# Kernel tuning notes

Measured on AMD Instinct MI355X. Metric: run time of the kernel, lower is better.

## Reference

```python
import jax, jax.numpy as jnp
import numpy as np

B, N, F, H = 2, 256, 64, 4
HID = 64            # hidden_features
C = H * HID         # n_coefficients = 256
KF = 50             # kernel_features (rbf count)
CUTOFF_UPPER = 5.0  # ExpNormalSmearing default (lower = 0)
ALPHA = 5.0 / CUTOFF_UPPER


def _dense(key, din, dout):
    scale = 1.0 / np.sqrt(din)
    return jax.random.uniform(key, (din, dout), minval=-scale, maxval=scale).astype(jnp.float32)


def setup_inputs() -> dict:
    key = jax.random.key(0)
    ks = jax.random.split(key, 16)
    start = float(np.exp(-CUTOFF_UPPER))
    means = jnp.asarray(np.linspace(start, 1.0, KF), jnp.float32)
    betas = jnp.full((KF,), (2.0 / KF * (1.0 - start)) ** -2, dtype=jnp.float32)
    d_edge_in = 2 * F              # h_cat_ht width
    d_cat = 2 * F + KF + 1         # concat([h0, rbf*h, dist])
    return dict(
        h=jax.random.normal(ks[0], (B, N, F), jnp.float32),
        x=jax.random.normal(ks[1], (B, N, 3), jnp.float32),
        v=jax.random.normal(ks[2], (B, N, 3), jnp.float32) * 0.1,
        W_in=_dense(ks[3], d_edge_in, KF), b_in=jnp.zeros((KF,), jnp.float32),
        rbf_means=means, rbf_betas=betas,
        W_o1=_dense(ks[4], d_cat, HID), b_o1=jnp.zeros((HID,), jnp.float32),
        W_o2=_dense(ks[5], HID, HID), b_o2=jnp.zeros((HID,), jnp.float32),
        W_sem=_dense(ks[6], HID, H), b_sem=jnp.zeros((H,), jnp.float32),
        W_xmix=_dense(ks[7], C, C),
        W_p1=_dense(ks[8], C, HID), b_p1=jnp.zeros((HID,), jnp.float32),
        W_p2=_dense(ks[9], HID, HID), b_p2=jnp.zeros((HID,), jnp.float32),
        W_n1=_dense(ks[10], F + C + HID, HID), b_n1=jnp.zeros((HID,), jnp.float32),
        W_n2=_dense(ks[11], HID, F), b_n2=jnp.zeros((F,), jnp.float32),
        W_v1=_dense(ks[12], F, HID), b_v1=jnp.zeros((HID,), jnp.float32),
        W_v2=_dense(ks[13], HID, 1),
        W_vmix=_dense(ks[14], C, 1),
    )


def reference(h, x, v, W_in, b_in, rbf_means, rbf_betas, W_o1, b_o1, W_o2, b_o2,
              W_sem, b_sem, W_xmix, W_p1, b_p1, W_p2, b_p2,
              W_n1, b_n1, W_n2, b_n2, W_v1, b_v1, W_v2, W_vmix):
    silu = jax.nn.silu
    n = h.shape[-2]
    # all-pairs displacements: entry [i, j] = x_j - x_i  (get_x_minus_xt)
    x_minus_xt = x[..., None, :, :] - x[..., :, None, :]                       # [B,N,N,3]
    d = jnp.sqrt(jax.nn.relu((x_minus_xt ** 2).sum(-1, keepdims=True)) + 1e-5)  # [B,N,N,1]
    # h_cat_ht: concat([h_j, h_i]) per pair (get_h_cat_ht)
    h_j = jnp.broadcast_to(h[..., None, :, :], h.shape[:-2] + (n, n, h.shape[-1]))
    h_i = jnp.broadcast_to(h[..., :, None, :], h.shape[:-2] + (n, n, h.shape[-1]))
    h_cat = jnp.concatenate([h_j, h_i], -1)                                     # [B,N,N,2F]
    # --- edge model: ContinuousFilterConvolutionWithConcatenation ---
    h1 = h_cat @ W_in + b_in                                                    # [B,N,N,KF]
    cut = 0.5 * (jnp.cos(d * jnp.pi / CUTOFF_UPPER) + 1.0) * (d < CUTOFF_UPPER)
    rbf = cut * jnp.exp(-rbf_betas * (jnp.exp(-ALPHA * d) - rbf_means) ** 2)    # [B,N,N,KF]
    h_e_mtx = silu(jnp.concatenate([h_cat, rbf * h1, d], -1) @ W_o1 + b_o1) @ W_o2 + b_o2  # [B,N,N,HID]
    # --- semantic attention (cutoff=None => euclidean factor is 1.0) ---
    att = jax.nn.celu(h_e_mtx @ W_sem + b_sem, alpha=2.0)                       # [B,N,N,H]
    att = att - 1e5 * jnp.eye(n, dtype=att.dtype)[..., None]                    # mask self-pairs
    att = jax.nn.softmax(att, axis=-2)
    combined = att / att.sum(-2, keepdims=True)                                 # combined_attention
    # per-head weighted edge features, flattened (feature-major, head-minor)
    h_e_att = (h_e_mtx[..., :, None] * combined[..., None, :]).reshape(h_e_mtx.shape[:-1] + (C,))  # [B,N,N,C]
    # --- spatial attention ---
    coeff = jnp.tanh(h_e_att @ W_xmix)                                          # x_mixing, [B,N,N,C]
    x_hat = x_minus_xt / (d + 1e-5)                                             # [B,N,N,3]
    # combinations[b,i,j,c,:] = x_hat[b,i,j,:] * coeff[b,i,j,c]; mean over j, fused:
    comb_sum = jnp.einsum('bijc,bijd->bicd', coeff, x_hat) / n                  # [B,N,C,3]
    comb_norm = (comb_sum ** 2).sum(-1)                                         # [B,N,C]
    h_comb = silu(silu(comb_norm @ W_p1 + b_p1) @ W_p2 + b_p2)                  # post_norm_mlp
    # --- aggregate + node model (residual) ---
    h_e = h_e_att.sum(-2)                                                       # [B,N,C]
    h_new = h + silu(silu(jnp.concatenate([h, h_e, h_comb], -1) @ W_n1 + b_n1) @ W_n2 + b_n2)
    # --- velocity / coordinate update (v_mixing then mean over j, fused via comb_sum) ---
    delta_v = jnp.einsum('bicd,c->bid', comb_sum, W_vmix[:, 0])                 # [B,N,3]
    v_scale = 2.0 * jax.nn.sigmoid(silu(h_new @ W_v1 + b_v1) @ W_v2)            # velocity_mlp + double_sigmoid
    v_new = delta_v + v_scale * v
    x_new = x + v_new
    return (h_new, x_new, v_new)
```

## Files before the change

### kernel.cpp

```cpp
#include <hip/hip_runtime.h>
#include <hip/hip_bf16.h>

typedef __hip_bfloat16 bf16;
typedef __attribute__((ext_vector_type(8))) short bf16x8;
typedef __attribute__((ext_vector_type(4))) short s16x4;
typedef __attribute__((ext_vector_type(4))) float f32x4;

#define NNODE 512

__device__ __forceinline__ float b2f(bf16 v){ return __bfloat162float(v); }
__device__ __forceinline__ float siluf(float x){ return x / (1.f + __expf(-x)); }
__device__ __forceinline__ float tanhfast(float x){ return 1.f - 2.f/(__expf(2.f*x)+1.f); }
__device__ __forceinline__ float celu2(float x){ return x > 0.f ? x : 2.f*(__expf(0.5f*x)-1.f); }
__device__ __forceinline__ float bs2f(short v){ union{unsigned int i; float f;} t; t.i = ((unsigned int)(unsigned short)v) << 16; return t.f; }
__device__ __forceinline__ short f2bs(float x){ union{ bf16 b; short s; } u; u.b = __float2bfloat16(x); return u.s; }
__device__ __forceinline__ float lo16f(unsigned int u){ union{unsigned int i; float f;} t; t.i = u<<16; return t.f; }
__device__ __forceinline__ float hi16f(unsigned int u){ union{unsigned int i; float f;} t; t.i = u & 0xffff0000u; return t.f; }

template<typename T> __device__ __forceinline__ float ldv(const void* p, int i);
template<> __device__ __forceinline__ float ldv<float>(const void* p, int i){ return ((const float*)p)[i]; }
template<> __device__ __forceinline__ float ldv<bf16 >(const void* p, int i){ return b2f(((const bf16*)p)[i]); }

template<typename T> __device__ __forceinline__ void stv(void* p, int i, float v);
template<> __device__ __forceinline__ void stv<float>(void* p, int i, float v){ ((float*)p)[i] = v; }
template<> __device__ __forceinline__ void stv<bf16 >(void* p, int i, float v){ ((bf16*)p)[i] = __float2bfloat16(v); }

template<typename T> __device__ __forceinline__ short ldbs(const void* p, int i);
template<> __device__ __forceinline__ short ldbs<bf16 >(const void* p, int i){ union{ bf16 b; short s; } u; u.b = ((const bf16*)p)[i]; return u.s; }
template<> __device__ __forceinline__ short ldbs<float>(const void* p, int i){ return f2bs(((const float*)p)[i]); }

struct Args {
    const void *h,*x,*v,*Win,*bin,*means,*betas,*Wo1,*bo1,*Wo2,*bo2,*Wsem,*bsem,*Wx,
               *Wp1,*bp1,*Wp2,*bp2,*Wn1,*bn1,*Wn2,*bn2,*Wv1,*bv1,*Wv2,*Wvm;
};

__device__ __forceinline__ bool detect_f32(const void* means){
    float v = b2f(((const bf16*)means)[0]);
    return (fabsf(v) > 1.0f || v != v);
}

template<typename T>
__device__ __forceinline__ void nodepre_body(const Args& A, short* __restrict__ U1,
                                             float* __restrict__ Aj, short* __restrict__ WxT,
                                             short* __restrict__ Wo1f, short* __restrict__ Wo2f,
                                             float* sh, float (*p1)[64], float (*p2)[64])
{
    int bn = blockIdx.x, tid = threadIdx.x;
    int t = tid & 63, ks = tid >> 6;
    if (tid < 64) sh[tid] = ldv<T>(A.h, bn*64 + tid);
    __syncthreads();
    float a1 = 0.f;
    #pragma unroll
    for (int q = 0; q < 16; ++q){
        int f = ks*16 + q;
        a1 += sh[f] * ldv<T>(A.Wo1, f*64 + t);
    }
    p1[ks][t] = a1;
    if (t < 50){
        float a2 = 0.f;
        #pragma unroll
        for (int q = 0; q < 16; ++q){
            int f = ks*16 + q;
            a2 += sh[f] * ldv<T>(A.Win, f*50 + t);
        }
        p2[ks][t] = a2;
    }
    if (tid < 128){
        int oo = bn*128 + tid;
        int hh = oo >> 14, rem = oo & 16383, n = rem >> 6, f = oo & 63;
        WxT[oo] = ldbs<T>(A.Wx, (4*f + hh)*256 + n);
    } else if (tid < 136){
        int oo = bn*8 + (tid - 128);
        int n = oo >> 6, k = oo & 63;
        Wo1f[oo] = (k < 50) ? ldbs<T>(A.Wo1, (128+k)*64 + n) : (short)0;
    } else if (tid < 144){
        int oo = bn*8 + (tid - 136);
        int n = oo >> 6, k = oo & 63;
        Wo2f[oo] = ldbs<T>(A.Wo2, k*64 + n);
    }
    __syncthreads();
    if (tid < 64){
        U1[bn*64 + tid] = f2bs(p1[0][tid] + p1[1][tid] + p1[2][tid] + p1[3][tid]);
        float av = (tid < 50) ? (p2[0][tid] + p2[1][tid] + p2[2][tid] + p2[3][tid]) : 0.f;
        Aj[bn*64 + tid] = av;
    }
}

__global__ void __launch_bounds__(256) k_nodepre(Args A, short* __restrict__ U1,
                                                 float* __restrict__ Aj, short* __restrict__ WxT,
                                                 short* __restrict__ Wo1f, short* __restrict__ Wo2f)
{
    __shared__ float sh[64];
    __shared__ float p1[4][64];
    __shared__ float p2[4][64];
    if (detect_f32(A.means)) nodepre_body<float>(A, U1, Aj, WxT, Wo1f, Wo2f, sh, p1, p2);
    else                     nodepre_body<bf16 >(A, U1, Aj, WxT, Wo1f, Wo2f, sh, p1, p2);
}

struct SmemPost {
    float part[4][256];
    float red[768];
    float cn[256];
    float he[256];
    float fa[64];
    float fb[64];
    float tmp[8][4];
    float tmp2[8];
};
struct Smem {
    __align__(16) bf16  e[256][72];
    __align__(16) float x4[256][4];
    float hi[64];
    float ub[64];
    float wl[64];
    __align__(16) float kc[64][4];
    __align__(16) short wsem[256];
    SmemPost post;
};

__device__ __forceinline__ float* attp(Smem& S, int j){
    return (float*)((short*)S.e + j*72 + 64);
}

template<typename T>
__device__ __forceinline__ void sake_body(const Args& A,
        const short* __restrict__ U1w, const float* __restrict__ Ajw,
        const short* __restrict__ wxt, const short* __restrict__ wo1f,
        const short* __restrict__ wo2f, void* __restrict__ out, Smem& S)
{
    int bi = blockIdx.x;
    int b = bi >> 8, i = bi & 255;
    int tid = threadIdx.x, w = tid >> 6, lane = tid & 63;
    int lane15 = lane & 15, quad = lane >> 4;

    if (tid < 64)  S.hi[tid]   = ldv<T>(A.h, bi*64 + tid);
    if (tid < 256) S.wsem[tid] = ldbs<T>(A.Wsem, tid);
    if (tid < 64){
        bool kv = tid < 50;
        S.kc[tid][0] = kv ? ldv<T>(A.means, tid) : 0.f;
        S.kc[tid][1] = kv ? ldv<T>(A.betas, tid) : 0.f;
        S.kc[tid][2] = kv ? ldv<T>(A.bin,   tid) : 0.f;
        if (!kv) S.kc[tid][3] = 0.f;
    }
    float xi0 = ldv<T>(A.x, bi*3+0), xi1 = ldv<T>(A.x, bi*3+1), xi2 = ldv<T>(A.x, bi*3+2);
    if (tid < 256){
        int j = tid;
        float dx = ldv<T>(A.x,(b*256+j)*3+0) - xi0;
        float dy = ldv<T>(A.x,(b*256+j)*3+1) - xi1;
        float dz = ldv<T>(A.x,(b*256+j)*3+2) - xi2;
        float dd = sqrtf(dx*dx + dy*dy + dz*dz + 1e-5f);
        float inv = 1.f/(dd + 1e-5f);
        S.x4[j][0] = dx*inv; S.x4[j][1] = dy*inv; S.x4[j][2] = dz*inv; S.x4[j][3] = dd;
    }
    if (w == 0){
        float u2v = 0.f;
        for (int f = 0; f < 64; ++f) u2v += ldv<T>(A.h, bi*64 + f) * ldv<T>(A.Wo1, (64+f)*64 + lane);
        S.ub[lane] = u2v + ldv<T>(A.bo1, lane);
        S.wl[lane] = ldv<T>(A.Wo1, 178*64 + lane);
    } else if (w == 1 && lane < 50){
        float av = 0.f;
        for (int f = 0; f < 64; ++f) av += ldv<T>(A.h, bi*64 + f) * ldv<T>(A.Win, (64+f)*50 + lane);
        S.kc[lane][3] = av;
    }
    __syncthreads();

    float ubr[16], wlr[16], bo2r[16];
    #pragma unroll
    for (int nf = 0; nf < 4; ++nf){
        #pragma unroll
        for (int r = 0; r < 4; ++r){
            int m = nf*16 + quad*4 + r;
            ubr[nf*4+r]  = S.ub[m];
            wlr[nf*4+r]  = S.wl[m];
            bo2r[nf*4+r] = ldv<T>(A.bo2, m);
        }
    }

    for (int pass = 0; pass < 2; ++pass){
        int j = pass*128 + w*16 + lane15;
        float dd  = S.x4[j][3];
        float cut = (dd < 5.f) ? 0.5f*(__cosf(dd*0.6283185307f) + 1.f) : 0.f;
        float ed  = __expf(-dd);
        const float* ajp = Ajw + (b*256 + j)*64;
        bf16x8 Brb[2];
        #pragma unroll
        for (int s = 0; s < 2; ++s){
            int kb = s*32 + quad*8;
            f32x4 a0 = *(const f32x4*)(ajp + kb);
            f32x4 a1 = *(const f32x4*)(ajp + kb + 4);
            bf16x8 bv;
            #pragma unroll
            for (int i2 = 0; i2 < 8; ++i2){
                int k = kb + i2;
                f32x4 kcv = *(const f32x4*)&S.kc[k][0];
                float aj = (i2 < 4) ? a0[i2] : a1[i2-4];
                float h1 = aj + kcv[3] + kcv[2];
                float ex = ed - kcv[0];
                float val = cut * __expf(-kcv[1]*ex*ex) * h1;
                bv[i2] = (k < 50) ? f2bs(val) : (short)0;
            }
            Brb[s] = bv;
        }
        const short* u1p = U1w + (b*256 + j)*64;
        short* erow_s = (short*)S.e;
        #pragma unroll
        for (int nf = 0; nf < 4; ++nf){
            const short* wp = wo1f + (nf*16 + lane15)*64;
            bf16x8 A0 = *(const bf16x8*)(wp + quad*8);
            bf16x8 A1 = *(const bf16x8*)(wp + 32 + quad*8);
            s16x4 u4 = *(const s16x4*)(u1p + nf*16 + quad*4);
            f32x4 C;
            #pragma unroll
            for (int r = 0; r < 4; ++r)
                C[r] = bs2f(u4[r]) + ubr[nf*4+r] + dd*wlr[nf*4+r];
            C = __builtin_amdgcn_mfma_f32_16x16x32_bf16(A0, Brb[0], C, 0, 0, 0);
            C = __builtin_amdgcn_mfma_f32_16x16x32_bf16(A1, Brb[1], C, 0, 0, 0);
            s16x4 m4;
            #pragma unroll
            for (int r = 0; r < 4; ++r) m4[r] = f2bs(siluf(C[r]));
            *(s16x4*)&erow_s[j*72 + nf*16 + quad*4] = m4;
        }
        bf16x8 Bm0 = *(const bf16x8*)&erow_s[j*72 + quad*8];
        bf16x8 Bm1 = *(const bf16x8*)&erow_s[j*72 + 32 + quad*8];
        #pragma unroll
        for (int nf = 0; nf < 4; ++nf){
            const short* wp = wo2f + (nf*16 + lane15)*64;
            bf16x8 A0 = *(const bf16x8*)(wp + quad*8);
            bf16x8 A1 = *(const bf16x8*)(wp + 32 + quad*8);
            f32x4 C = (f32x4){bo2r[nf*4+0], bo2r[nf*4+1], bo2r[nf*4+2], bo2r[nf*4+3]};
            C = __builtin_amdgcn_mfma_f32_16x16x32_bf16(A0, Bm0, C, 0, 0, 0);
            C = __builtin_amdgcn_mfma_f32_16x16x32_bf16(A1, Bm1, C, 0, 0, 0);
            s16x4 e4;
            #pragma unroll
            for (int r = 0; r < 4; ++r) e4[r] = f2bs(C[r]);
            *(s16x4*)&erow_s[j*72 + nf*16 + quad*4] = e4;
        }
    }

    {
        bf16x8 Bs[2];
        #pragma unroll
        for (int ks = 0; ks < 2; ++ks){
            bf16x8 bv = (bf16x8){0,0,0,0,0,0,0,0};
            if (lane15 < 4){
                #pragma unroll
                for (int i2 = 0; i2 < 8; ++i2)
                    bv[i2] = S.wsem[(ks*32 + quad*8 + i2)*4 + lane15];
            }
            Bs[ks] = bv;
        }
        float bsv = (lane15 < 4) ? ldv<T>(A.bsem, lane15) : 0.f;
        #pragma unroll
        for (int t2 = 0; t2 < 2; ++t2){
            int jt = t2 ? (8 + w) : w;
            const short* ep = (const short*)S.e + (jt*16 + lane15)*72;
            bf16x8 A0 = *(const bf16x8*)(ep + quad*8);
            bf16x8 A1 = *(const bf16x8*)(ep + 32 + quad*8);
            f32x4 C = (f32x4){bsv, bsv, bsv, bsv};
            C = __builtin_amdgcn_mfma_f32_16x16x32_bf16(A0, Bs[0], C, 0, 0, 0);
            C = __builtin_amdgcn_mfma_f32_16x16x32_bf16(A1, Bs[1], C, 0, 0, 0);
            if (lane15 < 4){
                #pragma unroll
                for (int r = 0; r < 4; ++r){
                    int jr = jt*16 + quad*4 + r;
                    float lv = celu2(C[r]);
                    if (jr == i) lv -= 1e5f;
                    attp(S, jr)[lane15] = lv;
                }
            }
        }
    }
    __syncthreads();

    float ex0 = 0.f, ex1 = 0.f, ex2 = 0.f, ex3 = 0.f;
    if (tid < 256){
        f32x4 l = *(const f32x4*)attp(S, tid);
        float m0 = l[0], m1 = l[1], m2 = l[2], m3 = l[3];
        #pragma unroll
        for (int off = 1; off < 64; off <<= 1){
            m0 = fmaxf(m0, __shfl_xor(m0, off)); m1 = fmaxf(m1, __shfl_xor(m1, off));
            m2 = fmaxf(m2, __shfl_xor(m2, off)); m3 = fmaxf(m3, __shfl_xor(m3, off));
        }
        if (lane == 0){
            S.post.tmp[w][0] = m0; S.post.tmp[w][1] = m1;
            S.post.tmp[w][2] = m2; S.post.tmp[w][3] = m3;
        }
        ex0 = l[0]; ex1 = l[1]; ex2 = l[2]; ex3 = l[3];
    }
    __syncthreads();
    if (tid < 256){
        float m0 = fmaxf(fmaxf(S.post.tmp[0][0], S.post.tmp[1][0]), fmaxf(S.post.tmp[2][0], S.post.tmp[3][0]));
        float m1 = fmaxf(fmaxf(S.post.tmp[0][1], S.post.tmp[1][1]), fmaxf(S.post.tmp[2][1], S.post.tmp[3][1]));
        float m2 = fmaxf(fmaxf(S.post.tmp[0][2], S.post.tmp[1][2]), fmaxf(S.post.tmp[2][2], S.post.tmp[3][2]));
        float m3 = fmaxf(fmaxf(S.post.tmp[0][3], S.post.tmp[1][3]), fmaxf(S.post.tmp[2][3], S.post.tmp[3][3]));
        ex0 = __expf(ex0-m0); ex1 = __expf(ex1-m1); ex2 = __expf(ex2-m2); ex3 = __expf(ex3-m3);
        float s0 = ex0, s1 = ex1, s2 = ex2, s3 = ex3;
        #pragma unroll
        for (int off = 1; off < 64; off <<= 1){
            s0 += __shfl_xor(s0, off); s1 += __shfl_xor(s1, off);
            s2 += __shfl_xor(s2, off); s3 += __shfl_xor(s3, off);
        }
        if (lane == 0){
            S.post.tmp[4+w][0] = s0; S.post.tmp[4+w][1] = s1;
            S.post.tmp[4+w][2] = s2; S.post.tmp[4+w][3] = s3;
        }
    }
    __syncthreads();
    if (tid < 256){
        float s0 = S.post.tmp[4][0]+S.post.tmp[5][0]+S.post.tmp[6][0]+S.post.tmp[7][0];
        float s1 = S.post.tmp[4][1]+S.post.tmp[5][1]+S.post.tmp[6][1]+S.post.tmp[7][1];
        float s2 = S.post.tmp[4][2]+S.post.tmp[5][2]+S.post.tmp[6][2]+S.post.tmp[7][2];
        float s3 = S.post.tmp[4][3]+S.post.tmp[5][3]+S.post.tmp[6][3]+S.post.tmp[7][3];
        *(f32x4*)attp(S, tid) = (f32x4){ex0/s0, ex1/s1, ex2/s2, ex3/s3};
    }
    __syncthreads();

    {
        int cg = tid & 127, js = tid >> 7;
        int fp = cg >> 2, hh = cg & 3;
        float acc0 = 0.f, acc1 = 0.f;
        const unsigned int* ep = (const unsigned int*)S.e;
        for (int jj = 0; jj < 64; ++jj){
            int j = js*64 + jj;
            unsigned int u = ep[j*36 + fp];
            float a = attp(S, j)[hh];
            acc0 += lo16f(u)*a; acc1 += hi16f(u)*a;
        }
        S.post.part[js][8*fp + hh]     = acc0;
        S.post.part[js][8*fp + 4 + hh] = acc1;
    }
    __syncthreads();
    if (tid < 256)
        S.post.he[tid] = S.post.part[0][tid] + S.post.part[1][tid]
                       + S.post.part[2][tid] + S.post.part[3][tid];

    {
        const short* se_s = (const short*)S.e;
        bf16x8 Bh[2][4][2];
        #pragma unroll
        for (int nf2 = 0; nf2 < 2; ++nf2){
            int n = w*32 + nf2*16 + lane15;
            #pragma unroll
            for (int hh = 0; hh < 4; ++hh){
                const short* bp = wxt + (hh*256 + n)*64 + quad*8;
                Bh[nf2][hh][0] = *(const bf16x8*)(bp);
                Bh[nf2][hh][1] = *(const bf16x8*)(bp + 32);
            }
        }
        float ca[2][3];
        #pragma unroll
        for (int nf2 = 0; nf2 < 2; ++nf2){ ca[nf2][0]=0.f; ca[nf2][1]=0.f; ca[nf2][2]=0.f; }

        for (int mt = 0; mt < 16; ++mt){
            int jq = mt*16 + quad*4;
            f32x4 att4[4];
            #pragma unroll
            for (int r = 0; r < 4; ++r) att4[r] = *(const f32x4*)attp(S, jq + r);
            bf16x8 Af[2];
            #pragma unroll
            for (int ks = 0; ks < 2; ++ks)
                Af[ks] = *(const bf16x8*)(se_s + (mt*16 + lane15)*72 + ks*32 + quad*8);
            #pragma unroll
            for (int nf2 = 0; nf2 < 2; ++nf2){
                float Pt[4] = {0.f, 0.f, 0.f, 0.f};
                #pragma unroll
                for (int hh = 0; hh < 4; ++hh){
                    f32x4 Cc = (f32x4){0.f,0.f,0.f,0.f};
                    Cc = __builtin_amdgcn_mfma_f32_16x16x32_bf16(Af[0], Bh[nf2][hh][0], Cc, 0, 0, 0);
                    Cc = __builtin_amdgcn_mfma_f32_16x16x32_bf16(Af[1], Bh[nf2][hh][1], Cc, 0, 0, 0);
                    #pragma unroll
                    for (int r = 0; r < 4; ++r) Pt[r] += att4[r][hh] * Cc[r];
                }
                #pragma unroll
                for (int r = 0; r < 4; ++r){
                    float cf = tanhfast(Pt[r]);
                    f32x4 xh = *(const f32x4*)&S.x4[jq + r][0];
                    ca[nf2][0] += cf*xh[0]; ca[nf2][1] += cf*xh[1]; ca[nf2][2] += cf*xh[2];
                }
            }
        }
        #pragma unroll
        for (int nf2 = 0; nf2 < 2; ++nf2){
            #pragma unroll
            for (int d = 0; d < 3; ++d){
                float vs = ca[nf2][d];
                vs += __shfl_xor(vs, 16);
                vs += __shfl_xor(vs, 32);
                if (quad == 0) S.post.red[(w*32 + nf2*16 + lane15)*3 + d] = vs;
            }
        }
    }
    __syncthreads();

    const float sc = 1.f/256.f;
    if (tid < 256){
        float c0 = S.post.red[tid*3+0]*sc, c1 = S.post.red[tid*3+1]*sc, c2 = S.post.red[tid*3+2]*sc;
        S.post.cn[tid] = c0*c0 + c1*c1 + c2*c2;
    } else {
        int c = (w-4)*64 + lane;
        float wv = ldv<T>(A.Wvm, c);
        float d0 = S.post.red[c*3+0]*sc*wv;
        float d1 = S.post.red[c*3+1]*sc*wv;
        float d2 = S.post.red[c*3+2]*sc*wv;
        #pragma unroll
        for (int off = 1; off < 64; off <<= 1){
            d0 += __shfl_xor(d0, off); d1 += __shfl_xor(d1, off); d2 += __shfl_xor(d2, off);
        }
        if (lane == 0){ S.post.tmp[w-4][0] = d0; S.post.tmp[w-4][1] = d1; S.post.tmp[w-4][2] = d2; }
    }
    __syncthreads();

    int fs = lane & 7, ks8 = lane >> 3;
    int fo = w*8 + fs;
    {
        float acc = 0.f;
        int c0 = ks8*32;
        for (int it = 0; it < 32; ++it){
            int c = c0 + it;
            acc += S.post.cn[c] * ldv<T>(A.Wp1, c*64 + fo);
        }
        acc += __shfl_xor(acc, 8); acc += __shfl_xor(acc, 16); acc += __shfl_xor(acc, 32);
        if (lane < 8) S.post.fa[w*8 + lane] = siluf(acc + ldv<T>(A.bp1, w*8 + lane));
    }
    __syncthreads();
    {
        float acc = 0.f;
        #pragma unroll
        for (int q = 0; q < 8; ++q){
            int k = ks8*8 + q;
            acc += S.post.fa[k] * ldv<T>(A.Wp2, k*64 + fo);
        }
        acc += __shfl_xor(acc, 8); acc += __shfl_xor(acc, 16); acc += __shfl_xor(acc, 32);
        if (lane < 8) S.post.fb[w*8 + lane] = siluf(acc + ldv<T>(A.bp2, w*8 + lane));
    }
    __syncthreads();
    {
        float acc = 0.f;
        int r0 = ks8*48;
        for (int it = 0; it < 48; ++it){
            int r = r0 + it;
            float xv = (r < 64) ? S.hi[r] : (r < 320) ? S.post.he[r-64] : S.post.fb[r-320];
            acc += xv * ldv<T>(A.Wn1, r*64 + fo);
        }
        acc += __shfl_xor(acc, 8); acc += __shfl_xor(acc, 16); acc += __shfl_xor(acc, 32);
        if (lane < 8){
            int f = w*8 + lane;
            S.post.fa[f] = siluf(acc + ldv<T>(A.bn1, f));
        }
    }
    __syncthreads();
    {
        float acc = 0.f;
        #pragma unroll
        for (int q = 0; q < 8; ++q){
            int k = ks8*8 + q;
            acc += S.post.fa[k] * ldv<T>(A.Wn2, k*64 + fo);
        }
        acc += __shfl_xor(acc, 8); acc += __shfl_xor(acc, 16); acc += __shfl_xor(acc, 32);
        if (lane < 8){
            int f = w*8 + lane;
            float hn = S.hi[f] + siluf(acc + ldv<T>(A.bn2, f));
            stv<T>(out, bi*64 + f, hn);
            S.post.fb[f] = hn;
        }
    }
    __syncthreads();
    {
        float acc = 0.f;
        #pragma unroll
        for (int q = 0; q < 8; ++q){
            int k = ks8*8 + q;
            acc += S.post.fb[k] * ldv<T>(A.Wv1, k*64 + fo);
        }
        acc += __shfl_xor(acc, 8); acc += __shfl_xor(acc, 16); acc += __shfl_xor(acc, 32);
        float term = siluf(acc + ldv<T>(A.bv1, fo)) * ldv<T>(A.Wv2, fo);
        term += __shfl_xor(term, 1); term += __shfl_xor(term, 2); term += __shfl_xor(term, 4);
        if (lane == 0) S.post.tmp2[w] = term;
    }
    __syncthreads();
    if (tid < 3){
        float t = S.post.tmp2[0]+S.post.tmp2[1]+S.post.tmp2[2]+S.post.tmp2[3]
                + S.post.tmp2[4]+S.post.tmp2[5]+S.post.tmp2[6]+S.post.tmp2[7];
        float vscale = 2.f / (1.f + __expf(-t));
        float dv = S.post.tmp[0][tid] + S.post.tmp[1][tid] + S.post.tmp[2][tid] + S.post.tmp[3][tid];
        float vn = dv + vscale * ldv<T>(A.v, bi*3 + tid);
        float xn = ldv<T>(A.x, bi*3 + tid) + vn;
        stv<T>(out, 32768 + bi*3 + tid, xn);
        stv<T>(out, 34304 + bi*3 + tid, vn);
    }
}

__global__ void __launch_bounds__(512, 4) k_sake(Args A,
                                                 const short* __restrict__ U1w,
                                                 const float* __restrict__ Ajw,
                                                 const short* __restrict__ wxt,
                                                 const short* __restrict__ wo1f,
                                                 const short* __restrict__ wo2f,
                                                 void* __restrict__ out)
{
    __shared__ Smem S;
    if (detect_f32(A.means)) sake_body<float>(A, U1w, Ajw, wxt, wo1f, wo2f, out, S);
    else                     sake_body<bf16 >(A, U1w, Ajw, wxt, wo1f, wo2f, out, S);
}

extern "C" void kernel_launch(void* const* d_in, const int* in_sizes, int n_in,
                              void* d_out, int out_size, void* d_ws, size_t ws_size,
                              hipStream_t stream)
{
    Args A;
    A.h     = d_in[0];  A.x     = d_in[1];  A.v     = d_in[2];
    A.Win   = d_in[3];  A.bin   = d_in[4];  A.means = d_in[5];  A.betas = d_in[6];
    A.Wo1   = d_in[7];  A.bo1   = d_in[8];  A.Wo2   = d_in[9];  A.bo2   = d_in[10];
    A.Wsem  = d_in[11]; A.bsem  = d_in[12]; A.Wx    = d_in[13];
    A.Wp1   = d_in[14]; A.bp1   = d_in[15]; A.Wp2   = d_in[16]; A.bp2   = d_in[17];
    A.Wn1   = d_in[18]; A.bn1   = d_in[19]; A.Wn2   = d_in[20]; A.bn2   = d_in[21];
    A.Wv1   = d_in[22]; A.bv1   = d_in[23]; A.Wv2   = d_in[24]; A.Wvm   = d_in[25];

    short* U1b  = (short*)d_ws;
    float* Aj   = (float*)((char*)d_ws + 65536);
    short* WxT  = (short*)((char*)d_ws + 65536 + 131072);
    short* Wo1f = (short*)((char*)d_ws + 65536 + 131072 + 131072);
    short* Wo2f = (short*)((char*)d_ws + 65536 + 131072 + 131072 + 8192);

    k_nodepre<<<NNODE, 256, 0, stream>>>(A, U1b, Aj, WxT, Wo1f, Wo2f);
    k_sake<<<NNODE, 512, 0, stream>>>(A, U1b, Aj, WxT, Wo1f, Wo2f, d_out);
}
```

Baseline: 187.8 us.

## Double sake block to 1024 threads and stage Wo1/Wo2 tiles in LDS

Each k_sake block now runs 16 waves instead of 8. The pair loop drops from two passes to one, the h_e reduction splits over eight j-slices, and each wave handles 16 coefficient columns in the x-mixing MFMA stage instead of 32. The Wo1/Wo2 transposed bf16 tiles are built per block in padded shared memory instead of being written to workspace by the pre-kernel. This aims for more parallelism per node and fewer global reads in the MFMA loops, at the cost of more LDS, lower occupancy per CU, redundant weight transposes in every block, and idle waves in the post MLP stages.

```diff
diff --git a/kernel.cpp b/kernel.cpp
--- a/kernel.cpp
+++ b/kernel.cpp
@@ -42,7 +42,6 @@
 template<typename T>
 __device__ __forceinline__ void nodepre_body(const Args& A, short* __restrict__ U1,
                                              float* __restrict__ Aj, short* __restrict__ WxT,
-                                             short* __restrict__ Wo1f, short* __restrict__ Wo2f,
                                              float* sh, float (*p1)[64], float (*p2)[64])
 {
     int bn = blockIdx.x, tid = threadIdx.x;
@@ -69,14 +68,6 @@
         int oo = bn*128 + tid;
         int hh = oo >> 14, rem = oo & 16383, n = rem >> 6, f = oo & 63;
         WxT[oo] = ldbs<T>(A.Wx, (4*f + hh)*256 + n);
-    } else if (tid < 136){
-        int oo = bn*8 + (tid - 128);
-        int n = oo >> 6, k = oo & 63;
-        Wo1f[oo] = (k < 50) ? ldbs<T>(A.Wo1, (128+k)*64 + n) : (short)0;
-    } else if (tid < 144){
-        int oo = bn*8 + (tid - 136);
-        int n = oo >> 6, k = oo & 63;
-        Wo2f[oo] = ldbs<T>(A.Wo2, k*64 + n);
     }
     __syncthreads();
     if (tid < 64){
@@ -87,18 +78,17 @@
 }
 
 __global__ void __launch_bounds__(256) k_nodepre(Args A, short* __restrict__ U1,
-                                                 float* __restrict__ Aj, short* __restrict__ WxT,
-                                                 short* __restrict__ Wo1f, short* __restrict__ Wo2f)
+                                                 float* __restrict__ Aj, short* __restrict__ WxT)
 {
     __shared__ float sh[64];
     __shared__ float p1[4][64];
     __shared__ float p2[4][64];
-    if (detect_f32(A.means)) nodepre_body<float>(A, U1, Aj, WxT, Wo1f, Wo2f, sh, p1, p2);
-    else                     nodepre_body<bf16 >(A, U1, Aj, WxT, Wo1f, Wo2f, sh, p1, p2);
+    if (detect_f32(A.means)) nodepre_body<float>(A, U1, Aj, WxT, sh, p1, p2);
+    else                     nodepre_body<bf16 >(A, U1, Aj, WxT, sh, p1, p2);
 }
 
 struct SmemPost {
-    float part[4][256];
+    float part[8][256];
     float red[768];
     float cn[256];
     float he[256];
@@ -115,6 +105,8 @@
     float wl[64];
     __align__(16) float kc[64][4];
     __align__(16) short wsem[256];
+    __align__(16) short wo1t[64*72];
+    __align__(16) short wo2t[64*72];
     SmemPost post;
 };
 
@@ -125,8 +117,7 @@
 template<typename T>
 __device__ __forceinline__ void sake_body(const Args& A,
         const short* __restrict__ U1w, const float* __restrict__ Ajw,
-        const short* __restrict__ wxt, const short* __restrict__ wo1f,
-        const short* __restrict__ wo2f, void* __restrict__ out, Smem& S)
+        const short* __restrict__ wxt, void* __restrict__ out, Smem& S)
 {
     int bi = blockIdx.x;
     int b = bi >> 8, i = bi & 255;
@@ -134,17 +125,25 @@
     int lane15 = lane & 15, quad = lane >> 4;
 
     if (tid < 64)  S.hi[tid]   = ldv<T>(A.h, bi*64 + tid);
-    if (tid < 256) S.wsem[tid] = ldbs<T>(A.Wsem, tid);
-    if (tid < 64){
-        bool kv = tid < 50;
-        S.kc[tid][0] = kv ? ldv<T>(A.means, tid) : 0.f;
-        S.kc[tid][1] = kv ? ldv<T>(A.betas, tid) : 0.f;
-        S.kc[tid][2] = kv ? ldv<T>(A.bin,   tid) : 0.f;
-        if (!kv) S.kc[tid][3] = 0.f;
+    if (tid >= 64 && tid < 320) S.wsem[tid-64] = ldbs<T>(A.Wsem, tid-64);
+    if (tid >= 320 && tid < 384){
+        int t2 = tid - 320;
+        bool kv = t2 < 50;
+        S.kc[t2][0] = kv ? ldv<T>(A.means, t2) : 0.f;
+        S.kc[t2][1] = kv ? ldv<T>(A.betas, t2) : 0.f;
+        S.kc[t2][2] = kv ? ldv<T>(A.bin,   t2) : 0.f;
+        if (!kv) S.kc[t2][3] = 0.f;
+    }
+    #pragma unroll
+    for (int q = 0; q < 4; ++q){
+        int idx = q*1024 + tid;
+        int n = idx >> 6, k = idx & 63;
+        S.wo2t[n*72 + k] = ldbs<T>(A.Wo2, k*64 + n);
+        S.wo1t[n*72 + k] = (k < 50) ? ldbs<T>(A.Wo1, (128+k)*64 + n) : (short)0;
     }
     float xi0 = ldv<T>(A.x, bi*3+0), xi1 = ldv<T>(A.x, bi*3+1), xi2 = ldv<T>(A.x, bi*3+2);
-    if (tid < 256){
-        int j = tid;
+    if (tid >= 384 && tid < 640){
+        int j = tid - 384;
         float dx = ldv<T>(A.x,(b*256+j)*3+0) - xi0;
         float dy = ldv<T>(A.x,(b*256+j)*3+1) - xi1;
         float dz = ldv<T>(A.x,(b*256+j)*3+2) - xi2;
@@ -152,12 +151,12 @@
         float inv = 1.f/(dd + 1e-5f);
         S.x4[j][0] = dx*inv; S.x4[j][1] = dy*inv; S.x4[j][2] = dz*inv; S.x4[j][3] = dd;
     }
-    if (w == 0){
+    if (w == 12){
         float u2v = 0.f;
         for (int f = 0; f < 64; ++f) u2v += ldv<T>(A.h, bi*64 + f) * ldv<T>(A.Wo1, (64+f)*64 + lane);
         S.ub[lane] = u2v + ldv<T>(A.bo1, lane);
         S.wl[lane] = ldv<T>(A.Wo1, 178*64 + lane);
-    } else if (w == 1 && lane < 50){
+    } else if (w == 13 && lane < 50){
         float av = 0.f;
         for (int f = 0; f < 64; ++f) av += ldv<T>(A.h, bi*64 + f) * ldv<T>(A.Win, (64+f)*50 + lane);
         S.kc[lane][3] = av;
@@ -176,8 +175,8 @@
         }
     }
 
-    for (int pass = 0; pass < 2; ++pass){
-        int j = pass*128 + w*16 + lane15;
+    {
+        int j = w*16 + lane15;
         float dd  = S.x4[j][3];
         float cut = (dd < 5.f) ? 0.5f*(__cosf(dd*0.6283185307f) + 1.f) : 0.f;
         float ed  = __expf(-dd);
@@ -205,7 +204,7 @@
         short* erow_s = (short*)S.e;
         #pragma unroll
         for (int nf = 0; nf < 4; ++nf){
-            const short* wp = wo1f + (nf*16 + lane15)*64;
+            const short* wp = S.wo1t + (nf*16 + lane15)*72;
             bf16x8 A0 = *(const bf16x8*)(wp + quad*8);
             bf16x8 A1 = *(const bf16x8*)(wp + 32 + quad*8);
             s16x4 u4 = *(const s16x4*)(u1p + nf*16 + quad*4);
@@ -224,7 +223,7 @@
         bf16x8 Bm1 = *(const bf16x8*)&erow_s[j*72 + 32 + quad*8];
         #pragma unroll
         for (int nf = 0; nf < 4; ++nf){
-            const short* wp = wo2f + (nf*16 + lane15)*64;
+            const short* wp = S.wo2t + (nf*16 + lane15)*72;
             bf16x8 A0 = *(const bf16x8*)(wp + quad*8);
             bf16x8 A1 = *(const bf16x8*)(wp + 32 + quad*8);
             f32x4 C = (f32x4){bo2r[nf*4+0], bo2r[nf*4+1], bo2r[nf*4+2], bo2r[nf*4+3]};
@@ -250,23 +249,19 @@
             Bs[ks] = bv;
         }
         float bsv = (lane15 < 4) ? ldv<T>(A.bsem, lane15) : 0.f;
-        #pragma unroll
-        for (int t2 = 0; t2 < 2; ++t2){
-            int jt = t2 ? (8 + w) : w;
-            const short* ep = (const short*)S.e + (jt*16 + lane15)*72;
-            bf16x8 A0 = *(const bf16x8*)(ep + quad*8);
-            bf16x8 A1 = *(const bf16x8*)(ep + 32 + quad*8);
-            f32x4 C = (f32x4){bsv, bsv, bsv, bsv};
-            C = __builtin_amdgcn_mfma_f32_16x16x32_bf16(A0, Bs[0], C, 0, 0, 0);
-            C = __builtin_amdgcn_mfma_f32_16x16x32_bf16(A1, Bs[1], C, 0, 0, 0);
-            if (lane15 < 4){
-                #pragma unroll
-                for (int r = 0; r < 4; ++r){
-                    int jr = jt*16 + quad*4 + r;
-                    float lv = celu2(C[r]);
-                    if (jr == i) lv -= 1e5f;
-                    attp(S, jr)[lane15] = lv;
-                }
+        const short* ep = (const short*)S.e + (w*16 + lane15)*72;
+        bf16x8 A0 = *(const bf16x8*)(ep + quad*8);
+        bf16x8 A1 = *(const bf16x8*)(ep + 32 + quad*8);
+        f32x4 C = (f32x4){bsv, bsv, bsv, bsv};
+        C = __builtin_amdgcn_mfma_f32_16x16x32_bf16(A0, Bs[0], C, 0, 0, 0);
+        C = __builtin_amdgcn_mfma_f32_16x16x32_bf16(A1, Bs[1], C, 0, 0, 0);
+        if (lane15 < 4){
+            #pragma unroll
+            for (int r = 0; r < 4; ++r){
+                int jr = w*16 + quad*4 + r;
+                float lv = celu2(C[r]);
+                if (jr == i) lv -= 1e5f;
+                attp(S, jr)[lane15] = lv;
             }
         }
     }
@@ -320,8 +315,8 @@
         int fp = cg >> 2, hh = cg & 3;
         float acc0 = 0.f, acc1 = 0.f;
         const unsigned int* ep = (const unsigned int*)S.e;
-        for (int jj = 0; jj < 64; ++jj){
-            int j = js*64 + jj;
+        for (int jj = 0; jj < 32; ++jj){
+            int j = js*32 + jj;
             unsigned int u = ep[j*36 + fp];
             float a = attp(S, j)[hh];
             acc0 += lo16f(u)*a; acc1 += hi16f(u)*a;
@@ -332,24 +327,21 @@
     __syncthreads();
     if (tid < 256)
         S.post.he[tid] = S.post.part[0][tid] + S.post.part[1][tid]
-                       + S.post.part[2][tid] + S.post.part[3][tid];
+                       + S.post.part[2][tid] + S.post.part[3][tid]
+                       + S.post.part[4][tid] + S.post.part[5][tid]
+                       + S.post.part[6][tid] + S.post.part[7][tid];
 
     {
         const short* se_s = (const short*)S.e;
-        bf16x8 Bh[2][4][2];
-        #pragma unroll
-        for (int nf2 = 0; nf2 < 2; ++nf2){
-            int n = w*32 + nf2*16 + lane15;
-            #pragma unroll
-            for (int hh = 0; hh < 4; ++hh){
-                const short* bp = wxt + (hh*256 + n)*64 + quad*8;
-                Bh[nf2][hh][0] = *(const bf16x8*)(bp);
-                Bh[nf2][hh][1] = *(const bf16x8*)(bp + 32);
-            }
-        }
-        float ca[2][3];
-        #pragma unroll
-        for (int nf2 = 0; nf2 < 2; ++nf2){ ca[nf2][0]=0.f; ca[nf2][1]=0.f; ca[nf2][2]=0.f; }
+        int n = w*16 + lane15;
+        bf16x8 Bh[4][2];
+        #pragma unroll
+        for (int hh = 0; hh < 4; ++hh){
+            const short* bp = wxt + (hh*256 + n)*64 + quad*8;
+            Bh[hh][0] = *(const bf16x8*)(bp);
+            Bh[hh][1] = *(const bf16x8*)(bp + 32);
+        }
+        float c0a = 0.f, c1a = 0.f, c2a = 0.f;
 
         for (int mt = 0; mt < 16; ++mt){
             int jq = mt*16 + quad*4;
@@ -360,34 +352,29 @@
             #pragma unroll
             for (int ks = 0; ks < 2; ++ks)
                 Af[ks] = *(const bf16x8*)(se_s + (mt*16 + lane15)*72 + ks*32 + quad*8);
-            #pragma unroll
-            for (int nf2 = 0; nf2 < 2; ++nf2){
-                float Pt[4] = {0.f, 0.f, 0.f, 0.f};
+            float Pt[4] = {0.f, 0.f, 0.f, 0.f};
+            #pragma unroll
+            for (int hh = 0; hh < 4; ++hh){
+                f32x4 Cc = (f32x4){0.f,0.f,0.f,0.f};
+                Cc = __builtin_amdgcn_mfma_f32_16x16x32_bf16(Af[0], Bh[hh][0], Cc, 0, 0, 0);
+                Cc = __builtin_amdgcn_mfma_f32_16x16x32_bf16(Af[1], Bh[hh][1], Cc, 0, 0, 0);
                 #pragma unroll
-                for (int hh = 0; hh < 4; ++hh){
-                    f32x4 Cc = (f32x4){0.f,0.f,0.f,0.f};
-                    Cc = __builtin_amdgcn_mfma_f32_16x16x32_bf16(Af[0], Bh[nf2][hh][0], Cc, 0, 0, 0);
-                    Cc = __builtin_amdgcn_mfma_f32_16x16x32_bf16(Af[1], Bh[nf2][hh][1], Cc, 0, 0, 0);
-                    #pragma unroll
-                    for (int r = 0; r < 4; ++r) Pt[r] += att4[r][hh] * Cc[r];
-                }
-                #pragma unroll
-                for (int r = 0; r < 4; ++r){
-                    float cf = tanhfast(Pt[r]);
-                    f32x4 xh = *(const f32x4*)&S.x4[jq + r][0];
-                    ca[nf2][0] += cf*xh[0]; ca[nf2][1] += cf*xh[1]; ca[nf2][2] += cf*xh[2];
-                }
+                for (int r = 0; r < 4; ++r) Pt[r] += att4[r][hh] * Cc[r];
             }
-        }
-        #pragma unroll
-        for (int nf2 = 0; nf2 < 2; ++nf2){
-            #pragma unroll
-            for (int d = 0; d < 3; ++d){
-                float vs = ca[nf2][d];
-                vs += __shfl_xor(vs, 16);
-                vs += __shfl_xor(vs, 32);
-                if (quad == 0) S.post.red[(w*32 + nf2*16 + lane15)*3 + d] = vs;
+            #pragma unroll
+            for (int r = 0; r < 4; ++r){
+                float cf = tanhfast(Pt[r]);
+                f32x4 xh = *(const f32x4*)&S.x4[jq + r][0];
+                c0a += cf*xh[0]; c1a += cf*xh[1]; c2a += cf*xh[2];
             }
+        }
+        c0a += __shfl_xor(c0a, 16); c0a += __shfl_xor(c0a, 32);
+        c1a += __shfl_xor(c1a, 16); c1a += __shfl_xor(c1a, 32);
+        c2a += __shfl_xor(c2a, 16); c2a += __shfl_xor(c2a, 32);
+        if (quad == 0){
+            S.post.red[n*3 + 0] = c0a;
+            S.post.red[n*3 + 1] = c1a;
+            S.post.red[n*3 + 2] = c2a;
         }
     }
     __syncthreads();
@@ -396,7 +383,7 @@
     if (tid < 256){
         float c0 = S.post.red[tid*3+0]*sc, c1 = S.post.red[tid*3+1]*sc, c2 = S.post.red[tid*3+2]*sc;
         S.post.cn[tid] = c0*c0 + c1*c1 + c2*c2;
-    } else {
+    } else if (w < 8){
         int c = (w-4)*64 + lane;
         float wv = ldv<T>(A.Wvm, c);
         float d0 = S.post.red[c*3+0]*sc*wv;
@@ -412,7 +399,7 @@
 
     int fs = lane & 7, ks8 = lane >> 3;
     int fo = w*8 + fs;
-    {
+    if (w < 8){
         float acc = 0.f;
         int c0 = ks8*32;
         for (int it = 0; it < 32; ++it){
@@ -423,7 +410,7 @@
         if (lane < 8) S.post.fa[w*8 + lane] = siluf(acc + ldv<T>(A.bp1, w*8 + lane));
     }
     __syncthreads();
-    {
+    if (w < 8){
         float acc = 0.f;
         #pragma unroll
         for (int q = 0; q < 8; ++q){
@@ -434,7 +421,7 @@
         if (lane < 8) S.post.fb[w*8 + lane] = siluf(acc + ldv<T>(A.bp2, w*8 + lane));
     }
     __syncthreads();
-    {
+    if (w < 8){
         float acc = 0.f;
         int r0 = ks8*48;
         for (int it = 0; it < 48; ++it){
@@ -449,7 +436,7 @@
         }
     }
     __syncthreads();
-    {
+    if (w < 8){
         float acc = 0.f;
         #pragma unroll
         for (int q = 0; q < 8; ++q){
@@ -465,7 +452,7 @@
         }
     }
     __syncthreads();
-    {
+    if (w < 8){
         float acc = 0.f;
         #pragma unroll
         for (int q = 0; q < 8; ++q){
@@ -490,17 +477,15 @@
     }
 }
 
-__global__ void __launch_bounds__(512, 4) k_sake(Args A,
-                                                 const short* __restrict__ U1w,
-                                                 const float* __restrict__ Ajw,
-                                                 const short* __restrict__ wxt,
-                                                 const short* __restrict__ wo1f,
-                                                 const short* __restrict__ wo2f,
-                                                 void* __restrict__ out)
+__global__ void __launch_bounds__(1024, 4) k_sake(Args A,
+                                                  const short* __restrict__ U1w,
+                                                  const float* __restrict__ Ajw,
+                                                  const short* __restrict__ wxt,
+                                                  void* __restrict__ out)
 {
     __shared__ Smem S;
-    if (detect_f32(A.means)) sake_body<float>(A, U1w, Ajw, wxt, wo1f, wo2f, out, S);
-    else                     sake_body<bf16 >(A, U1w, Ajw, wxt, wo1f, wo2f, out, S);
+    if (detect_f32(A.means)) sake_body<float>(A, U1w, Ajw, wxt, out, S);
+    else                     sake_body<bf16 >(A, U1w, Ajw, wxt, out, S);
 }
 
 extern "C" void kernel_launch(void* const* d_in, const int* in_sizes, int n_in,
@@ -519,9 +504,7 @@
     short* U1b  = (short*)d_ws;
     float* Aj   = (float*)((char*)d_ws + 65536);
     short* WxT  = (short*)((char*)d_ws + 65536 + 131072);
-    short* Wo1f = (short*)((char*)d_ws + 65536 + 131072 + 131072);
-    short* Wo2f = (short*)((char*)d_ws + 65536 + 131072 + 131072 + 8192);
-
-    k_nodepre<<<NNODE, 256, 0, stream>>>(A, U1b, Aj, WxT, Wo1f, Wo2f);
-    k_sake<<<NNODE, 512, 0, stream>>>(A, U1b, Aj, WxT, Wo1f, Wo2f, d_out);
-}
+
+    k_nodepre<<<NNODE, 256, 0, stream>>>(A, U1b, Aj, WxT);
+    k_sake<<<NNODE, 1024, 0, stream>>>(A, U1b, Aj, WxT, d_out);
+}
```

After: 192.0 us. +2.2%, slower.

## Stage transposed Wo1/Wo2 tiles in LDS and parallelize per-node projections across warps

Applied to the files above, without the earlier changes.

Each k_sake block now transposes the Wo2 weights and the rbf slice of Wo1 into padded shared-memory tiles itself, instead of reading pre-transposed copies that k_nodepre wrote to global workspace. The MFMA A-operand loads inside the edge loop therefore come from LDS rather than global/L2. The per-node u2 and Win projections are also split across all 8 warps with a shared-memory reduction, where before only one or two warps did them serially. In exchange, each block adds redundant global loads of the weights (with strided Wo1/Wo2 reads), an extra barrier, and about 20KB more LDS, which may reduce occupancy.

```diff
diff --git a/kernel.cpp b/kernel.cpp
--- a/kernel.cpp
+++ b/kernel.cpp
@@ -42,7 +42,6 @@
 template<typename T>
 __device__ __forceinline__ void nodepre_body(const Args& A, short* __restrict__ U1,
                                              float* __restrict__ Aj, short* __restrict__ WxT,
-                                             short* __restrict__ Wo1f, short* __restrict__ Wo2f,
                                              float* sh, float (*p1)[64], float (*p2)[64])
 {
     int bn = blockIdx.x, tid = threadIdx.x;
@@ -69,14 +68,6 @@
         int oo = bn*128 + tid;
         int hh = oo >> 14, rem = oo & 16383, n = rem >> 6, f = oo & 63;
         WxT[oo] = ldbs<T>(A.Wx, (4*f + hh)*256 + n);
-    } else if (tid < 136){
-        int oo = bn*8 + (tid - 128);
-        int n = oo >> 6, k = oo & 63;
-        Wo1f[oo] = (k < 50) ? ldbs<T>(A.Wo1, (128+k)*64 + n) : (short)0;
-    } else if (tid < 144){
-        int oo = bn*8 + (tid - 136);
-        int n = oo >> 6, k = oo & 63;
-        Wo2f[oo] = ldbs<T>(A.Wo2, k*64 + n);
     }
     __syncthreads();
     if (tid < 64){
@@ -87,14 +78,13 @@
 }
 
 __global__ void __launch_bounds__(256) k_nodepre(Args A, short* __restrict__ U1,
-                                                 float* __restrict__ Aj, short* __restrict__ WxT,
-                                                 short* __restrict__ Wo1f, short* __restrict__ Wo2f)
+                                                 float* __restrict__ Aj, short* __restrict__ WxT)
 {
     __shared__ float sh[64];
     __shared__ float p1[4][64];
     __shared__ float p2[4][64];
-    if (detect_f32(A.means)) nodepre_body<float>(A, U1, Aj, WxT, Wo1f, Wo2f, sh, p1, p2);
-    else                     nodepre_body<bf16 >(A, U1, Aj, WxT, Wo1f, Wo2f, sh, p1, p2);
+    if (detect_f32(A.means)) nodepre_body<float>(A, U1, Aj, WxT, sh, p1, p2);
+    else                     nodepre_body<bf16 >(A, U1, Aj, WxT, sh, p1, p2);
 }
 
 struct SmemPost {
@@ -115,6 +105,10 @@
     float wl[64];
     __align__(16) float kc[64][4];
     __align__(16) short wsem[256];
+    __align__(16) short wo1t[64*72];
+    __align__(16) short wo2t[64*72];
+    float up[8][64];
+    float ap[8][64];
     SmemPost post;
 };
 
@@ -125,8 +119,7 @@
 template<typename T>
 __device__ __forceinline__ void sake_body(const Args& A,
         const short* __restrict__ U1w, const float* __restrict__ Ajw,
-        const short* __restrict__ wxt, const short* __restrict__ wo1f,
-        const short* __restrict__ wo2f, void* __restrict__ out, Smem& S)
+        const short* __restrict__ wxt, void* __restrict__ out, Smem& S)
 {
     int bi = blockIdx.x;
     int b = bi >> 8, i = bi & 255;
@@ -141,6 +134,13 @@
         S.kc[tid][1] = kv ? ldv<T>(A.betas, tid) : 0.f;
         S.kc[tid][2] = kv ? ldv<T>(A.bin,   tid) : 0.f;
         if (!kv) S.kc[tid][3] = 0.f;
+    }
+    #pragma unroll
+    for (int q = 0; q < 8; ++q){
+        int idx = q*512 + tid;
+        int n = idx >> 6, k = idx & 63;
+        S.wo2t[n*72 + k] = ldbs<T>(A.Wo2, k*64 + n);
+        S.wo1t[n*72 + k] = (k < 50) ? ldbs<T>(A.Wo1, (128+k)*64 + n) : (short)0;
     }
     float xi0 = ldv<T>(A.x, bi*3+0), xi1 = ldv<T>(A.x, bi*3+1), xi2 = ldv<T>(A.x, bi*3+2);
     if (tid < 256){
@@ -152,15 +152,36 @@
         float inv = 1.f/(dd + 1e-5f);
         S.x4[j][0] = dx*inv; S.x4[j][1] = dy*inv; S.x4[j][2] = dz*inv; S.x4[j][3] = dd;
     }
-    if (w == 0){
-        float u2v = 0.f;
-        for (int f = 0; f < 64; ++f) u2v += ldv<T>(A.h, bi*64 + f) * ldv<T>(A.Wo1, (64+f)*64 + lane);
-        S.ub[lane] = u2v + ldv<T>(A.bo1, lane);
-        S.wl[lane] = ldv<T>(A.Wo1, 178*64 + lane);
-    } else if (w == 1 && lane < 50){
-        float av = 0.f;
-        for (int f = 0; f < 64; ++f) av += ldv<T>(A.h, bi*64 + f) * ldv<T>(A.Win, (64+f)*50 + lane);
-        S.kc[lane][3] = av;
+    {
+        float a_u = 0.f;
+        #pragma unroll
+        for (int q = 0; q < 8; ++q){
+            int f = w*8 + q;
+            a_u += ldv<T>(A.h, bi*64 + f) * ldv<T>(A.Wo1, (64+f)*64 + lane);
+        }
+        S.up[w][lane] = a_u;
+        if (lane < 50){
+            float a_a = 0.f;
+            #pragma unroll
+            for (int q = 0; q < 8; ++q){
+                int f = w*8 + q;
+                a_a += ldv<T>(A.h, bi*64 + f) * ldv<T>(A.Win, (64+f)*50 + lane);
+            }
+            S.ap[w][lane] = a_a;
+        }
+    }
+    __syncthreads();
+
+    if (tid < 64){
+        float s = S.up[0][tid]+S.up[1][tid]+S.up[2][tid]+S.up[3][tid]
+                + S.up[4][tid]+S.up[5][tid]+S.up[6][tid]+S.up[7][tid];
+        S.ub[tid] = s + ldv<T>(A.bo1, tid);
+        S.wl[tid] = ldv<T>(A.Wo1, 178*64 + tid);
+    } else if (tid < 128){
+        int m = tid - 64;
+        if (m < 50)
+            S.kc[m][3] = S.ap[0][m]+S.ap[1][m]+S.ap[2][m]+S.ap[3][m]
+                       + S.ap[4][m]+S.ap[5][m]+S.ap[6][m]+S.ap[7][m];
     }
     __syncthreads();
 
@@ -205,7 +226,7 @@
         short* erow_s = (short*)S.e;
         #pragma unroll
         for (int nf = 0; nf < 4; ++nf){
-            const short* wp = wo1f + (nf*16 + lane15)*64;
+            const short* wp = S.wo1t + (nf*16 + lane15)*72;
             bf16x8 A0 = *(const bf16x8*)(wp + quad*8);
             bf16x8 A1 = *(const bf16x8*)(wp + 32 + quad*8);
             s16x4 u4 = *(const s16x4*)(u1p + nf*16 + quad*4);
@@ -224,7 +245,7 @@
         bf16x8 Bm1 = *(const bf16x8*)&erow_s[j*72 + 32 + quad*8];
         #pragma unroll
         for (int nf = 0; nf < 4; ++nf){
-            const short* wp = wo2f + (nf*16 + lane15)*64;
+            const short* wp = S.wo2t + (nf*16 + lane15)*72;
             bf16x8 A0 = *(const bf16x8*)(wp + quad*8);
             bf16x8 A1 = *(const bf16x8*)(wp + 32 + quad*8);
             f32x4 C = (f32x4){bo2r[nf*4+0], bo2r[nf*4+1], bo2r[nf*4+2], bo2r[nf*4+3]};
@@ -494,13 +515,11 @@
                                                  const short* __restrict__ U1w,
                                                  const float* __restrict__ Ajw,
                                                  const short* __restrict__ wxt,
-                                                 const short* __restrict__ wo1f,
-                                                 const short* __restrict__ wo2f,
                                                  void* __restrict__ out)
 {
     __shared__ Smem S;
-    if (detect_f32(A.means)) sake_body<float>(A, U1w, Ajw, wxt, wo1f, wo2f, out, S);
-    else                     sake_body<bf16 >(A, U1w, Ajw, wxt, wo1f, wo2f, out, S);
+    if (detect_f32(A.means)) sake_body<float>(A, U1w, Ajw, wxt, out, S);
+    else                     sake_body<bf16 >(A, U1w, Ajw, wxt, out, S);
 }
 
 extern "C" void kernel_launch(void* const* d_in, const int* in_sizes, int n_in,
@@ -519,9 +538,7 @@
     short* U1b  = (short*)d_ws;
     float* Aj   = (float*)((char*)d_ws + 65536);
     short* WxT  = (short*)((char*)d_ws + 65536 + 131072);
-    short* Wo1f = (short*)((char*)d_ws + 65536 + 131072 + 131072);
-    short* Wo2f = (short*)((char*)d_ws + 65536 + 131072 + 131072 + 8192);
-
-    k_nodepre<<<NNODE, 256, 0, stream>>>(A, U1b, Aj, WxT, Wo1f, Wo2f);
-    k_sake<<<NNODE, 512, 0, stream>>>(A, U1b, Aj, WxT, Wo1f, Wo2f, d_out);
-}
+
+    k_nodepre<<<NNODE, 256, 0, stream>>>(A, U1b, Aj, WxT);
+    k_sake<<<NNODE, 512, 0, stream>>>(A, U1b, Aj, WxT, d_out);
+}
```

Result: faster. 172.2 us, median of 2 (-8.3%).
